# Performance work log

Measured on AMD Instinct MI355X. Metric: run time of the kernel, lower is better.

Reference implementation:

```python
import jax, jax.numpy as jnp
import numpy as np

NEG_SLOPE = 0.01  # torch F.leaky_relu default

def _leaky(x):
    return jnp.where(x >= 0, x, NEG_SLOPE * x)

def _gcn(x, W, b, src, dst, w, n):
    # GCNConv(add_self_loops=False, normalize=False):
    # h = x @ W; out[dst] += w * h[src]; out += b
    h = x @ W
    agg = jax.ops.segment_sum(w[:, None] * h[src], dst, num_segments=n)
    return agg + b

def setup_inputs() -> dict:
    key = jax.random.key(0)
    ks = jax.random.split(key, 10)
    N, E, IN, HID, OUT, B = 100000, 300000, 256, 256, 256, 128
    features = jax.random.normal(ks[0], (N, IN), dtype=jnp.float32)
    values = jax.random.uniform(ks[1], (E,), dtype=jnp.float32)
    s = 1.0 / np.sqrt(IN)
    W1 = jax.random.normal(ks[2], (IN, HID), dtype=jnp.float32) * s
    b1 = jnp.zeros((HID,), dtype=jnp.float32)
    W2 = jax.random.normal(ks[3], (HID + IN, OUT), dtype=jnp.float32) * (1.0 / np.sqrt(HID + IN))
    b2 = jnp.zeros((OUT,), dtype=jnp.float32)
    Wl = jax.random.normal(ks[4], (HID + OUT, IN), dtype=jnp.float32) * (1.0 / np.sqrt(HID + OUT))
    bl = jnp.zeros((IN,), dtype=jnp.float32)
    adjs = jax.random.randint(ks[5], (2, E), 0, N, dtype=jnp.int64)
    batch = jnp.sort(jax.random.randint(ks[6], (N,), 0, B, dtype=jnp.int64))
    root_idx = jax.random.randint(ks[7], (B,), 0, N, dtype=jnp.int64)
    return {"features": features, "values": values, "W1": W1, "b1": b1,
            "W2": W2, "b2": b2, "Wl": Wl, "bl": bl,
            "adjs": adjs, "batch": batch, "root_idx": root_idx}

def reference(features, values, W1, b1, W2, b2, Wl, bl, adjs, batch, root_idx):
    N = features.shape[0]
    src, dst = adjs[0], adjs[1]
    f1 = features  # [N, in]
    h = _gcn(f1, W1, b1, src, dst, values, N)  # conv1 -> [N, hid]
    f2 = h
    # root_extend: per-batch broadcast of root features == gather f1[root_idx[batch]]
    root1 = f1[root_idx[batch]]  # [N, in]
    x = _leaky(jnp.concatenate([h, root1], axis=1))
    # dropout is identity at inference
    x = _gcn(x, W2, b2, src, dst, values, N)  # conv2 -> [N, out]
    x = _leaky(x)
    root2 = f2[root_idx[batch]]  # [N, hid]
    x = jnp.concatenate([x, root2], axis=1)
    return _leaky(x @ Wl + bl)  # [N, in]
```

## Files before the change

### kernel.cpp

```cpp
#include <hip/hip_runtime.h>

typedef short short8 __attribute__((ext_vector_type(8)));
typedef float floatx4 __attribute__((ext_vector_type(4)));

#define LEAKY(v) ((v) >= 0.0f ? (v) : 0.01f * (v))

constexpr int D = 256;

__device__ __forceinline__ short f2bf(float x) {
  unsigned u = __float_as_uint(x);
  u += 0x7fffu + ((u >> 16) & 1u);
  return (short)(u >> 16);
}
__device__ __forceinline__ float bf2f(short s) {
  return __uint_as_float(((unsigned)(unsigned short)s) << 16);
}

__global__ void transpose_w(const float* __restrict__ W1,
                            const float* __restrict__ W2,
                            const float* __restrict__ Wl,
                            short* __restrict__ Wt) {
  __shared__ float t[32][33];
  const float* src = (blockIdx.z == 0) ? W1 : (blockIdx.z == 1) ? W2 : Wl;
  short* dst = Wt + (size_t)blockIdx.z * D * D;
  int tx = threadIdx.x, ty = threadIdx.y;
  t[ty][tx] = src[(size_t)(blockIdx.y * 32 + ty) * D + blockIdx.x * 32 + tx];
  __syncthreads();
  dst[(size_t)(blockIdx.x * 32 + ty) * D + blockIdx.y * 32 + tx] =
      f2bf(t[tx][ty]);
}

template <bool A_F32, bool ADD_ROW, bool FINAL>
__global__ __launch_bounds__(256) void gemm_mfma(
    const void* __restrict__ Avoid, const short* __restrict__ Wt,
    const float* __restrict__ R, const int* __restrict__ batch,
    const float* __restrict__ bias, void* __restrict__ Cvoid, int M) {
  __shared__ __align__(16) short As[64 * 72];
  __shared__ __align__(16) short Bs[256 * 72];
  const int tid = threadIdx.x;
  const int l = tid & 63, w = tid >> 6, lm = l & 15, q = l >> 4;
  const int rowBase = blockIdx.x * 64;

  floatx4 acc[4][4];
#pragma unroll
  for (int i = 0; i < 4; i++)
#pragma unroll
    for (int j = 0; j < 4; j++) acc[i][j] = (floatx4){0.f, 0.f, 0.f, 0.f};

  const int arow = tid >> 2;
  const int akseg = (tid & 3) * 16;

  for (int k0 = 0; k0 < D; k0 += 64) {
    {
      int grow = rowBase + arow;
      if (A_F32) {
        short8 s0 = {0, 0, 0, 0, 0, 0, 0, 0}, s1 = {0, 0, 0, 0, 0, 0, 0, 0};
        if (grow < M) {
          const float* ap = (const float*)Avoid + (size_t)grow * D + k0 + akseg;
          float4 v0 = ((const float4*)ap)[0];
          float4 v1 = ((const float4*)ap)[1];
          float4 v2 = ((const float4*)ap)[2];
          float4 v3 = ((const float4*)ap)[3];
          s0[0] = f2bf(v0.x); s0[1] = f2bf(v0.y); s0[2] = f2bf(v0.z); s0[3] = f2bf(v0.w);
          s0[4] = f2bf(v1.x); s0[5] = f2bf(v1.y); s0[6] = f2bf(v1.z); s0[7] = f2bf(v1.w);
          s1[0] = f2bf(v2.x); s1[1] = f2bf(v2.y); s1[2] = f2bf(v2.z); s1[3] = f2bf(v2.w);
          s1[4] = f2bf(v3.x); s1[5] = f2bf(v3.y); s1[6] = f2bf(v3.z); s1[7] = f2bf(v3.w);
        }
        *(short8*)(As + arow * 72 + akseg) = s0;
        *(short8*)(As + arow * 72 + akseg + 8) = s1;
      } else {
        uint4 u0 = {0, 0, 0, 0}, u1 = {0, 0, 0, 0};
        if (grow < M) {
          const uint4* ap =
              (const uint4*)((const short*)Avoid + (size_t)grow * D + k0 + akseg);
          u0 = ap[0];
          u1 = ap[1];
        }
        *(uint4*)(As + arow * 72 + akseg) = u0;
        *(uint4*)(As + arow * 72 + akseg + 8) = u1;
      }
    }
    {
      const uint4* wp = (const uint4*)(Wt + (size_t)tid * D + k0);
#pragma unroll
      for (int x = 0; x < 8; x++) *(uint4*)(Bs + tid * 72 + x * 8) = wp[x];
    }
    __syncthreads();
#pragma unroll
    for (int kk = 0; kk < 64; kk += 32) {
      short8 a[4], b[4];
#pragma unroll
      for (int i = 0; i < 4; i++)
        a[i] = *(const short8*)(As + (i * 16 + lm) * 72 + kk + q * 8);
#pragma unroll
      for (int j = 0; j < 4; j++)
        b[j] = *(const short8*)(Bs + (w * 64 + j * 16 + lm) * 72 + kk + q * 8);
#pragma unroll
      for (int i = 0; i < 4; i++)
#pragma unroll
        for (int j = 0; j < 4; j++)
          acc[i][j] = __builtin_amdgcn_mfma_f32_16x16x32_bf16(a[i], b[j],
                                                              acc[i][j], 0, 0, 0);
    }
    __syncthreads();
  }

#pragma unroll
  for (int i = 0; i < 4; i++) {
#pragma unroll
    for (int r = 0; r < 4; r++) {
      int row = rowBase + i * 16 + q * 4 + r;
      if (row < M) {
        int rb = 0;
        if (ADD_ROW) rb = batch[row];
        if (!FINAL) {
          short* C = (short*)Cvoid;
#pragma unroll
          for (int j = 0; j < 4; j++) {
            int col = w * 64 + j * 16 + lm;
            float c = acc[i][j][r];
            if (ADD_ROW) c += R[(size_t)rb * D + col];
            C[(size_t)row * D + col] = f2bf(c);
          }
        } else {
          float* C = (float*)Cvoid;
#pragma unroll
          for (int j = 0; j < 4; j++) {
            int col = w * 64 + j * 16 + lm;
            float c = acc[i][j][r];
            if (ADD_ROW) c += R[(size_t)rb * D + col];
            c += bias[col];
            c = LEAKY(c);
            C[(size_t)row * D + col] = c;
          }
        }
      }
    }
  }
}

__global__ void count_dst(const int* __restrict__ dst, int* __restrict__ offs,
                          int E) {
  int e = blockIdx.x * 256 + threadIdx.x;
  if (e < E) atomicAdd(&offs[dst[e]], 1);
}

__global__ void scan_blocks(int* __restrict__ offs, int* __restrict__ bsums,
                            int n) {
  __shared__ int tmp[256];
  int i = blockIdx.x * 256 + threadIdx.x;
  int v = (i < n) ? offs[i] : 0;
  tmp[threadIdx.x] = v;
  __syncthreads();
  for (int off = 1; off < 256; off <<= 1) {
    int t = (threadIdx.x >= off) ? tmp[threadIdx.x - off] : 0;
    __syncthreads();
    tmp[threadIdx.x] += t;
    __syncthreads();
  }
  if (i < n) offs[i] = tmp[threadIdx.x] - v;
  if (threadIdx.x == 255) bsums[blockIdx.x] = tmp[255];
}

__global__ void scan_sums(int* __restrict__ bs, int nb) {
  __shared__ int tmp[1024];
  int v = (threadIdx.x < nb) ? bs[threadIdx.x] : 0;
  tmp[threadIdx.x] = v;
  __syncthreads();
  for (int off = 1; off < 1024; off <<= 1) {
    int t = (threadIdx.x >= off) ? tmp[threadIdx.x - off] : 0;
    __syncthreads();
    tmp[threadIdx.x] += t;
    __syncthreads();
  }
  if (threadIdx.x < nb) bs[threadIdx.x] = tmp[threadIdx.x] - v;
}

__global__ void add_offsets(int* __restrict__ offs, const int* __restrict__ bs,
                            int n, int* __restrict__ cursor) {
  int i = blockIdx.x * 256 + threadIdx.x;
  if (i < n) {
    int o = offs[i] + bs[blockIdx.x];
    offs[i] = o;
    cursor[i] = o;
  }
}

__global__ void fill_buckets(const int* __restrict__ src,
                             const int* __restrict__ dst,
                             const float* __restrict__ vals,
                             int* __restrict__ cursor, int* __restrict__ esrc,
                             float* __restrict__ ew, int E) {
  int e = blockIdx.x * 256 + threadIdx.x;
  if (e < E) {
    int p = atomicAdd(&cursor[dst[e]], 1);
    esrc[p] = src[e];
    ew[p] = vals[e];
  }
}

__global__ __launch_bounds__(256) void aggregate_bf(
    const short* __restrict__ H, const int* __restrict__ offs,
    const int* __restrict__ esrc, const float* __restrict__ ew,
    const float* __restrict__ bias, short* __restrict__ out, int N, int E) {
  int node = blockIdx.x * 4 + (threadIdx.x >> 6);
  if (node >= N) return;
  int lane = threadIdx.x & 63;
  int beg = offs[node];
  int end = (node == N - 1) ? E : offs[node + 1];
  float a0 = 0.f, a1 = 0.f, a2 = 0.f, a3 = 0.f;
  for (int i = beg; i < end; i++) {
    int s = esrc[i];
    float wv = ew[i];
    uint2 pk = ((const uint2*)(H + (size_t)s * D))[lane];
    a0 += wv * bf2f((short)(pk.x & 0xffff));
    a1 += wv * bf2f((short)(pk.x >> 16));
    a2 += wv * bf2f((short)(pk.y & 0xffff));
    a3 += wv * bf2f((short)(pk.y >> 16));
  }
  float4 b = ((const float4*)bias)[lane];
  a0 = LEAKY(a0 + b.x);
  a1 = LEAKY(a1 + b.y);
  a2 = LEAKY(a2 + b.z);
  a3 = LEAKY(a3 + b.w);
  uint2 o;
  o.x = (unsigned)(unsigned short)f2bf(a0) |
        ((unsigned)(unsigned short)f2bf(a1) << 16);
  o.y = (unsigned)(unsigned short)f2bf(a2) |
        ((unsigned)(unsigned short)f2bf(a3) << 16);
  ((uint2*)(out + (size_t)node * D))[lane] = o;
}

__global__ void root_gemm1(const float* __restrict__ X,
                           const int* __restrict__ root_idx,
                           const float* __restrict__ W2,
                           float* __restrict__ R1) {
  __shared__ float a[D];
  int b = blockIdx.x, j = threadIdx.x;
  int r = root_idx[b];
  a[j] = LEAKY(X[(size_t)r * D + j]);
  __syncthreads();
  float acc = 0.f;
#pragma unroll 8
  for (int k = 0; k < D; k++) acc += a[k] * W2[(size_t)(D + k) * D + j];
  R1[b * D + j] = acc;
}

__global__ void root_gemm2(const short* __restrict__ H,
                           const int* __restrict__ root_idx,
                           const int* __restrict__ offs,
                           const int* __restrict__ esrc,
                           const float* __restrict__ ew,
                           const float* __restrict__ b1,
                           const float* __restrict__ Wl, float* __restrict__ R2,
                           int N, int E) {
  __shared__ float a[D];
  int b = blockIdx.x, j = threadIdx.x;
  int r = root_idx[b];
  int beg = offs[r], end = (r == N - 1) ? E : offs[r + 1];
  float acc = b1[j];
  for (int e = beg; e < end; e++)
    acc += ew[e] * bf2f(H[(size_t)esrc[e] * D + j]);
  a[j] = acc;
  __syncthreads();
  float s = 0.f;
#pragma unroll 8
  for (int k = 0; k < D; k++) s += a[k] * Wl[(size_t)(D + k) * D + j];
  R2[b * D + j] = s;
}

extern "C" void kernel_launch(void* const* d_in, const int* in_sizes, int n_in,
                              void* d_out, int out_size, void* d_ws,
                              size_t ws_size, hipStream_t stream) {
  const float* features = (const float*)d_in[0];
  const float* values   = (const float*)d_in[1];
  const float* W1 = (const float*)d_in[2];
  const float* b1 = (const float*)d_in[3];
  const float* W2 = (const float*)d_in[4];
  const float* b2 = (const float*)d_in[5];
  const float* Wl = (const float*)d_in[6];
  const float* bl = (const float*)d_in[7];
  const int* adjs = (const int*)d_in[8];
  const int* batch = (const int*)d_in[9];
  const int* root_idx = (const int*)d_in[10];

  const int N = in_sizes[0] / D;
  const int E = in_sizes[1];
  const int B = in_sizes[10];
  const int* srcI = adjs;
  const int* dstI = adjs + E;

  short* bf0 = (short*)d_ws;
  short* bf1 = bf0 + (size_t)N * D;
  short* Wt = bf1 + (size_t)N * D;
  float* R1 = (float*)(Wt + (size_t)3 * D * D);
  float* R2 = R1 + (size_t)B * D;
  float* ew = R2 + (size_t)B * D;
  int* offs = (int*)(ew + E);
  int* cursor = offs + N;
  int* esrc = cursor + N;
  int* bsums = esrc + E;

  const int nb = (N + 255) / 256;

  hipMemsetAsync(offs, 0, (size_t)N * sizeof(int), stream);
  count_dst<<<(E + 255) / 256, 256, 0, stream>>>(dstI, offs, E);
  scan_blocks<<<nb, 256, 0, stream>>>(offs, bsums, N);
  scan_sums<<<1, 1024, 0, stream>>>(bsums, nb);
  add_offsets<<<nb, 256, 0, stream>>>(offs, bsums, N, cursor);
  fill_buckets<<<(E + 255) / 256, 256, 0, stream>>>(srcI, dstI, values, cursor,
                                                    esrc, ew, E);

  transpose_w<<<dim3(8, 8, 3), dim3(32, 32), 0, stream>>>(W1, W2, Wl, Wt);

  const int ggrid = (N + 63) / 64;
  const int aggGrid = (N + 3) / 4;

  gemm_mfma<true, false, false><<<ggrid, 256, 0, stream>>>(
      features, Wt, nullptr, nullptr, nullptr, bf0, N);

  aggregate_bf<<<aggGrid, 256, 0, stream>>>(bf0, offs, esrc, ew, b1, bf1, N, E);

  root_gemm1<<<B, 256, 0, stream>>>(features, root_idx, W2, R1);
  root_gemm2<<<B, 256, 0, stream>>>(bf0, root_idx, offs, esrc, ew, b1, Wl, R2,
                                    N, E);

  gemm_mfma<false, true, false><<<ggrid, 256, 0, stream>>>(
      bf1, Wt + (size_t)D * D, R1, batch, nullptr, bf0, N);

  aggregate_bf<<<aggGrid, 256, 0, stream>>>(bf0, offs, esrc, ew, b2, bf1, N, E);

  gemm_mfma<false, true, true><<<ggrid, 256, 0, stream>>>(
      bf1, Wt + (size_t)2 * D * D, R2, batch, bl, (float*)d_out, N);
}
```

Measured before the change: 504.0 us.

## Load GEMM operand fragments directly from global memory, dropping LDS staging

New measurement: 580.7 us. 1.15x slower.

```diff
diff --git a/kernel.cpp b/kernel.cpp
--- a/kernel.cpp
+++ b/kernel.cpp
@@ -35,8 +35,6 @@
     const void* __restrict__ Avoid, const short* __restrict__ Wt,
     const float* __restrict__ R, const int* __restrict__ batch,
     const float* __restrict__ bias, void* __restrict__ Cvoid, int M) {
-  __shared__ __align__(16) short As[64 * 72];
-  __shared__ __align__(16) short Bs[256 * 72];
   const int tid = threadIdx.x;
   const int l = tid & 63, w = tid >> 6, lm = l & 15, q = l >> 4;
   const int rowBase = blockIdx.x * 64;
@@ -47,62 +45,44 @@
 #pragma unroll
     for (int j = 0; j < 4; j++) acc[i][j] = (floatx4){0.f, 0.f, 0.f, 0.f};
 
-  const int arow = tid >> 2;
-  const int akseg = (tid & 3) * 16;
-
-  for (int k0 = 0; k0 < D; k0 += 64) {
-    {
-      int grow = rowBase + arow;
-      if (A_F32) {
-        short8 s0 = {0, 0, 0, 0, 0, 0, 0, 0}, s1 = {0, 0, 0, 0, 0, 0, 0, 0};
-        if (grow < M) {
-          const float* ap = (const float*)Avoid + (size_t)grow * D + k0 + akseg;
-          float4 v0 = ((const float4*)ap)[0];
-          float4 v1 = ((const float4*)ap)[1];
-          float4 v2 = ((const float4*)ap)[2];
-          float4 v3 = ((const float4*)ap)[3];
-          s0[0] = f2bf(v0.x); s0[1] = f2bf(v0.y); s0[2] = f2bf(v0.z); s0[3] = f2bf(v0.w);
-          s0[4] = f2bf(v1.x); s0[5] = f2bf(v1.y); s0[6] = f2bf(v1.z); s0[7] = f2bf(v1.w);
-          s1[0] = f2bf(v2.x); s1[1] = f2bf(v2.y); s1[2] = f2bf(v2.z); s1[3] = f2bf(v2.w);
-          s1[4] = f2bf(v3.x); s1[5] = f2bf(v3.y); s1[6] = f2bf(v3.z); s1[7] = f2bf(v3.w);
-        }
-        *(short8*)(As + arow * 72 + akseg) = s0;
-        *(short8*)(As + arow * 72 + akseg + 8) = s1;
-      } else {
-        uint4 u0 = {0, 0, 0, 0}, u1 = {0, 0, 0, 0};
-        if (grow < M) {
-          const uint4* ap =
-              (const uint4*)((const short*)Avoid + (size_t)grow * D + k0 + akseg);
-          u0 = ap[0];
-          u1 = ap[1];
-        }
-        *(uint4*)(As + arow * 72 + akseg) = u0;
-        *(uint4*)(As + arow * 72 + akseg + 8) = u1;
+  int arow[4];
+#pragma unroll
+  for (int i = 0; i < 4; i++) {
+    int r0 = rowBase + i * 16 + lm;
+    arow[i] = (r0 < M) ? r0 : (M - 1);
+  }
+  const short* bbase = Wt + (size_t)(w * 64 + lm) * D + q * 8;
+
+#pragma unroll
+  for (int k0 = 0; k0 < D; k0 += 32) {
+    short8 a[4], b[4];
+    if (A_F32) {
+      const float* Af = (const float*)Avoid;
+#pragma unroll
+      for (int i = 0; i < 4; i++) {
+        const float* ap = Af + (size_t)arow[i] * D + k0 + q * 8;
+        float4 v0 = ((const float4*)ap)[0];
+        float4 v1 = ((const float4*)ap)[1];
+        short8 s;
+        s[0] = f2bf(v0.x); s[1] = f2bf(v0.y); s[2] = f2bf(v0.z); s[3] = f2bf(v0.w);
+        s[4] = f2bf(v1.x); s[5] = f2bf(v1.y); s[6] = f2bf(v1.z); s[7] = f2bf(v1.w);
+        a[i] = s;
       }
+    } else {
+      const short* Ab = (const short*)Avoid;
+#pragma unroll
+      for (int i = 0; i < 4; i++)
+        a[i] = *(const short8*)(Ab + (size_t)arow[i] * D + k0 + q * 8);
     }
-    {
-      const uint4* wp = (const uint4*)(Wt + (size_t)tid * D + k0);
-#pragma unroll
-      for (int x = 0; x < 8; x++) *(uint4*)(Bs + tid * 72 + x * 8) = wp[x];
-    }
-    __syncthreads();
-#pragma unroll
-    for (int kk = 0; kk < 64; kk += 32) {
-      short8 a[4], b[4];
-#pragma unroll
-      for (int i = 0; i < 4; i++)
-        a[i] = *(const short8*)(As + (i * 16 + lm) * 72 + kk + q * 8);
+#pragma unroll
+    for (int j = 0; j < 4; j++)
+      b[j] = *(const short8*)(bbase + (size_t)j * 16 * D + k0);
+#pragma unroll
+    for (int i = 0; i < 4; i++)
 #pragma unroll
       for (int j = 0; j < 4; j++)
-        b[j] = *(const short8*)(Bs + (w * 64 + j * 16 + lm) * 72 + kk + q * 8);
-#pragma unroll
-      for (int i = 0; i < 4; i++)
-#pragma unroll
-        for (int j = 0; j < 4; j++)
-          acc[i][j] = __builtin_amdgcn_mfma_f32_16x16x32_bf16(a[i], b[j],
-                                                              acc[i][j], 0, 0, 0);
-    }
-    __syncthreads();
+        acc[i][j] = __builtin_amdgcn_mfma_f32_16x16x32_bf16(a[i], b[j],
+                                                            acc[i][j], 0, 0, 0);
   }
 
 #pragma unroll
```
